# Optimization experiments

Measured on AMD Instinct MI355X. Metric: run time of the kernel, lower is better.

## Reference

```python
import jax, jax.numpy as jnp
import numpy as np

B, L = 4, 1024
V, D, H, NL = 32000, 256, 4, 8
S, DC, DI, NTYPES = 16, 4, 512, 5  # d_state, d_conv, d_inner=expand*d_model
NM, NA = 6, 2  # mamba blocks (layers 0,1,2,4,5,6), attention blocks (layers 3,7)


def layernorm(x, g, b):
    m = x.mean(-1, keepdims=True)
    v = x.var(-1, keepdims=True)
    return (x - m) / jnp.sqrt(v + 1e-5) * g + b


def mamba_block(x, g, b, in_w, conv_w, conv_b, xproj_w, dt_w, dt_b, A_log, Dp, out_w):
    res = x
    xn = layernorm(x, g, b)
    xz = xn @ in_w.T                          # [B,L,2*DI]
    xb, z = jnp.split(xz, 2, axis=-1)
    # depthwise causal conv1d (torch pads both sides then truncates to L == left-pad only)
    xc = jnp.transpose(xb, (0, 2, 1))         # [B,DI,L]
    xc = jax.lax.conv_general_dilated(xc, conv_w, (1,), [(DC - 1, 0)], feature_group_count=DI)
    xc = xc + conv_b[None, :, None]
    xb = jax.nn.silu(jnp.transpose(xc, (0, 2, 1)))  # [B,L,DI]
    A = -jnp.exp(A_log)                        # [DI,S]
    Bm, Cm = jnp.split(xb @ xproj_w.T, 2, axis=-1)  # each [B,L,S]
    dt = jax.nn.softplus(xb @ dt_w.T + dt_b)   # [B,L,DI]

    def step(h, inp):
        dt_t, B_t, C_t, x_t = inp              # [B,DI],[B,S],[B,S],[B,DI]
        A_bar = jnp.exp(dt_t[:, :, None] * A)  # [B,DI,S]
        h = A_bar * h + (dt_t * x_t)[:, :, None] * B_t[:, None, :]
        y = (h * C_t[:, None, :]).sum(-1) + Dp * x_t
        return h, y

    h0 = jnp.zeros((x.shape[0], DI, S), x.dtype)
    xs = (jnp.swapaxes(dt, 0, 1), jnp.swapaxes(Bm, 0, 1), jnp.swapaxes(Cm, 0, 1), jnp.swapaxes(xb, 0, 1))
    _, ys = jax.lax.scan(step, h0, xs)         # ys: [L,B,DI]
    y = jnp.swapaxes(ys, 0, 1) * jax.nn.silu(z)
    return y @ out_w.T + res


def attn_block(x, ts, mask, g, b, qkv_w, out_w, decay, ffg, ffb, ff1, ff2):
    Bs, Lq, Dm = x.shape
    dh = Dm // H
    res = x
    xn = layernorm(x, g, b)
    qkv = (xn @ qkv_w.T).reshape(Bs, Lq, 3, H, dh)
    q, k, v = qkv[:, :, 0], qkv[:, :, 1], qkv[:, :, 2]   # [B,L,H,dh]
    attn = jnp.einsum('bqhd,bkhd->bhqk', q, k) * dh ** -0.5
    t_diff = jnp.abs(ts[:, :, None] - ts[:, None, :])[:, None] / 24.0   # [B,1,L,L]
    attn = attn - jax.nn.softplus(decay)[None, :, None, None] * t_diff
    causal = jnp.triu(jnp.ones((Lq, Lq), bool), 1)
    attn = jnp.where(causal[None, None], -jnp.inf, attn)
    attn = jnp.where((mask == 0)[:, None, None, :], -jnp.inf, attn)
    attn = jax.nn.softmax(attn, axis=-1)       # dropout inactive (eval)
    out = jnp.einsum('bhqk,bkhd->bqhd', attn, v).reshape(Bs, Lq, Dm)
    x = res + out @ out_w.T
    xn2 = layernorm(x, ffg, ffb)
    return x + jax.nn.silu(xn2 @ ff1.T) @ ff2.T


def setup_inputs():
    key = jax.random.key(0)
    ks = iter(jax.random.split(key, 64))
    rn = lambda shape, s=0.02: jax.random.normal(next(ks), shape, jnp.float32) * s
    A_init = jnp.log(jnp.tile(jnp.arange(1, S + 1, dtype=jnp.float32)[None, None, :], (NM, DI, 1)))
    return dict(
        token_ids=jax.random.randint(next(ks), (B, L), 0, V, jnp.int32),
        token_types=jax.random.randint(next(ks), (B, L), 0, NTYPES, jnp.int32),
        timestamps=jax.random.uniform(next(ks), (B, L), jnp.float32) * 100.0,
        attention_mask=jnp.ones((B, L), jnp.int32),
        tok_emb=rn((V, D)).at[0].set(0.0),  # padding_idx=0
        type_emb=rn((NTYPES, D)),
        te_freq=rn((D // 2,), 0.01), te_phase=jnp.zeros((D // 2,)),
        te_w=rn((D, D)), te_b=jnp.zeros((D,)),
        m_norm_g=jnp.ones((NM, D)), m_norm_b=jnp.zeros((NM, D)),
        m_in_w=rn((NM, 2 * DI, D)),
        m_conv_w=rn((NM, DI, 1, DC)), m_conv_b=jnp.zeros((NM, DI)),
        m_xproj_w=rn((NM, 2 * S, DI)),
        m_dt_w=rn((NM, DI, DI)), m_dt_b=jnp.zeros((NM, DI)),
        m_Alog=A_init, m_D=jnp.ones((NM, DI)),
        m_out_w=rn((NM, D, DI)),
        a_norm_g=jnp.ones((NA, D)), a_norm_b=jnp.zeros((NA, D)),
        a_qkv_w=rn((NA, 3 * D, D)), a_out_w=rn((NA, D, D)),
        a_decay=jnp.full((NA, H), 0.01, jnp.float32),
        a_ffg=jnp.ones((NA, D)), a_ffb=jnp.zeros((NA, D)),
        a_ff1=rn((NA, 4 * D, D)), a_ff2=rn((NA, D, 4 * D)),
        f_g=jnp.ones((D,)), f_b=jnp.zeros((D,)),
        lm_w=rn((V, D)),
        re_w=rn((1, D)), re_b=jnp.zeros((1,)),
        mo_w=rn((1, D)), mo_b=jnp.zeros((1,)),
    )


def reference(token_ids, token_types, timestamps, attention_mask,
              tok_emb, type_emb, te_freq, te_phase, te_w, te_b,
              m_norm_g, m_norm_b, m_in_w, m_conv_w, m_conv_b, m_xproj_w,
              m_dt_w, m_dt_b, m_Alog, m_D, m_out_w,
              a_norm_g, a_norm_b, a_qkv_w, a_out_w, a_decay, a_ffg, a_ffb, a_ff1, a_ff2,
              f_g, f_b, lm_w, re_w, re_b, mo_w, mo_b):
    t = timestamps[..., None]
    freq = jax.nn.softplus(te_freq)
    enc = jnp.concatenate([jnp.sin(t * freq + te_phase), jnp.cos(t * freq + te_phase)], -1) @ te_w.T + te_b
    x = tok_emb[token_ids] + type_emb[token_types] + enc
    mi = ai = 0
    for i in range(NL):
        if (i + 1) % 4 == 0:
            x = attn_block(x, timestamps, attention_mask,
                           a_norm_g[ai], a_norm_b[ai], a_qkv_w[ai], a_out_w[ai], a_decay[ai],
                           a_ffg[ai], a_ffb[ai], a_ff1[ai], a_ff2[ai])
            ai += 1
        else:
            x = mamba_block(x, m_norm_g[mi], m_norm_b[mi], m_in_w[mi], m_conv_w[mi], m_conv_b[mi],
                            m_xproj_w[mi], m_dt_w[mi], m_dt_b[mi], m_Alog[mi], m_D[mi], m_out_w[mi])
            mi += 1
    x = layernorm(x, f_g, f_b)
    cls = x[:, 0, :]
    lm_logits = x @ lm_w.T
    readm = (cls @ re_w.T + re_b)[:, 0]
    mort = (cls @ mo_w.T + mo_b)[:, 0]
    return lm_logits, readm, mort
```

## Files before the change

kernel.cpp:

```cpp
#include <hip/hip_runtime.h>
#include <hip/hip_bf16.h>
#include <math.h>

#define BB 4
#define LL 1024
#define BL (BB*LL)
#define DD 256
#define VV 32000
#define HH 4
#define DH 64
#define SS 16
#define DCC 4
#define DII 512

typedef float f32x4 __attribute__((ext_vector_type(4)));
typedef short bh8  __attribute__((ext_vector_type(8)));
typedef unsigned short u16;

__device__ __forceinline__ float sp_f(float x) {
    return fmaxf(x, 0.f) + log1pf(expf(-fabsf(x)));
}
__device__ __forceinline__ float silu_f(float x) {
    return x / (1.f + expf(-x));
}
__device__ __forceinline__ short f2bf(float f) {
    __hip_bfloat16 h = __float2bfloat16(f);
    short s; __builtin_memcpy(&s, &h, 2); return s;
}
__device__ __forceinline__ float bf2f(u16 u) {
    unsigned v = ((unsigned)u) << 16;
    float f; __builtin_memcpy(&f, &v, 4); return f;
}

#define WB_TOT 5668864
#define LM_TOT 8192000
__global__ void cvtall_k(const float* __restrict__ te_w, const float* __restrict__ a_qkv,
                         const float* __restrict__ a_out, const float* __restrict__ a_ff1,
                         const float* __restrict__ a_ff2, const float* __restrict__ m_in,
                         const float* __restrict__ m_out, const float* __restrict__ m_dt,
                         const float* __restrict__ m_xp, const float* __restrict__ lm,
                         u16* __restrict__ dst, u16* __restrict__ dlm) {
    long i = ((long)blockIdx.x * 256 + threadIdx.x) * 4;
    const float* src; long off; u16* d; long doff;
    if (i >= WB_TOT) {
        long j = i - WB_TOT;
        if (j >= LM_TOT) return;
        src = lm; off = j; d = dlm; doff = j;
    } else {
        d = dst; doff = i;
        if      (i < 65536)   { src = te_w;  off = i; }
        else if (i < 458752)  { src = a_qkv; off = i - 65536; }
        else if (i < 589824)  { src = a_out; off = i - 458752; }
        else if (i < 1114112) { src = a_ff1; off = i - 589824; }
        else if (i < 1638400) { src = a_ff2; off = i - 1114112; }
        else if (i < 3211264) { src = m_in;  off = i - 1638400; }
        else if (i < 3997696) { src = m_out; off = i - 3211264; }
        else {
            long l = i - 3997696;
            int mi = (int)(l / 278528);
            long r = l - (long)mi * 278528;
            if (r < 262144) { src = m_dt + (long)mi * 262144; off = r; }
            else            { src = m_xp + (long)mi * 16384;  off = r - 262144; }
        }
    }
    float4 v = *(const float4*)(src + off);
    ushort4 u;
    u.x = (u16)f2bf(v.x); u.y = (u16)f2bf(v.y);
    u.z = (u16)f2bf(v.z); u.w = (u16)f2bf(v.w);
    *(ushort4*)(d + doff) = u;
}

__global__ void feat_k(const float* __restrict__ ts, const float* __restrict__ freq,
                       const float* __restrict__ phase, u16* __restrict__ feat) {
    int row = blockIdx.x, t = threadIdx.x;
    float tv = ts[row];
    int d = t & 127;
    float f = sp_f(freq[d]);
    float arg = tv * f + phase[d];
    feat[(size_t)row * DD + t] = (u16)f2bf((t < 128) ? sinf(arg) : cosf(arg));
}

__global__ void ln_k(const float* __restrict__ x, const float* __restrict__ g,
                     const float* __restrict__ bbias, u16* __restrict__ out) {
    __shared__ float red[8];
    int row = blockIdx.x, t = threadIdx.x;
    float v = x[(size_t)row * DD + t];
    float s = v;
    #pragma unroll
    for (int o = 32; o >= 1; o >>= 1) s += __shfl_xor(s, o);
    if ((t & 63) == 0) red[t >> 6] = s;
    __syncthreads();
    float mean = (red[0] + red[1] + red[2] + red[3]) * (1.f / 256.f);
    float d = v - mean;
    float s2 = d * d;
    #pragma unroll
    for (int o = 32; o >= 1; o >>= 1) s2 += __shfl_xor(s2, o);
    if ((t & 63) == 0) red[4 + (t >> 6)] = s2;
    __syncthreads();
    float var = (red[4] + red[5] + red[6] + red[7]) * (1.f / 256.f);
    out[(size_t)row * DD + t] = (u16)f2bf(d * rsqrtf(var + 1e-5f) * g[t] + bbias[t]);
}

template <int ACT, bool BOUT, bool VT>
__global__ __launch_bounds__(256) void lngemm_k(
    const float* __restrict__ X, const float* __restrict__ g, const float* __restrict__ bb,
    const u16* __restrict__ W, void* __restrict__ outv, u16* __restrict__ vt,
    int M, int N) {
    __shared__ __align__(16) char Abf[32768];
    __shared__ __align__(16) char Ws[8192];
    __shared__ float gs[256], bs[256];
    int tid = threadIdx.x;
    int bm = blockIdx.y * 64, bn = blockIdx.x * 64;
    gs[tid] = g[tid]; bs[tid] = bb[tid];

    int row = tid >> 2, part = tid & 3;
    const float* xr = X + (size_t)(bm + row) * 256 + part * 64;
    float4 vv[16];
    float s = 0.f, sq = 0.f;
    #pragma unroll
    for (int i = 0; i < 16; ++i) {
        vv[i] = *(const float4*)(xr + i * 4);
        s  += vv[i].x + vv[i].y + vv[i].z + vv[i].w;
        sq += vv[i].x * vv[i].x + vv[i].y * vv[i].y + vv[i].z * vv[i].z + vv[i].w * vv[i].w;
    }
    s += __shfl_xor(s, 1);  s += __shfl_xor(s, 2);
    sq += __shfl_xor(sq, 1); sq += __shfl_xor(sq, 2);
    float mean = s * (1.f / 256.f);
    float rstd = rsqrtf(sq * (1.f / 256.f) - mean * mean + 1e-5f);
    __syncthreads();
    #pragma unroll
    for (int i8 = 0; i8 < 8; ++i8) {
        bh8 p;
        #pragma unroll
        for (int j = 0; j < 8; ++j) {
            int e = i8 * 8 + j;
            float v = (j & 3) == 0 ? vv[e >> 2].x : (j & 3) == 1 ? vv[e >> 2].y
                    : (j & 3) == 2 ? vv[e >> 2].z : vv[e >> 2].w;
            int c = part * 64 + e;
            p[j] = f2bf((v - mean) * rstd * gs[c] + bs[c]);
        }
        *(bh8*)(Abf + (unsigned)((row * 512 + part * 128 + i8 * 16) ^ ((row & 7) << 4))) = p;
    }
    __syncthreads();

    int lane = tid & 63, wv = tid >> 6;
    int wm = wv >> 1, wn = wv & 1;
    int ro = lane & 15, kg = lane >> 4;
    f32x4 acc[2][2];
    #pragma unroll
    for (int i = 0; i < 2; ++i)
        #pragma unroll
        for (int j = 0; j < 2; ++j) acc[i][j] = (f32x4){0.f, 0.f, 0.f, 0.f};

    const u16* gw = W + (size_t)(bn + row) * 256 + part * 16;
    bool wvalid = (bn + row) < N;
    unsigned swb = (unsigned)(row * 128 + part * 32);
    unsigned sx  = (unsigned)((row & 7) << 4);
    for (int kk = 0; kk < 256; kk += 64) {
        if (kk) __syncthreads();
        bh8 w0 = {}, w1 = {};
        if (wvalid) { w0 = *(const bh8*)(gw + kk); w1 = *(const bh8*)(gw + kk + 8); }
        *(bh8*)(Ws + (swb ^ sx)) = w0;
        *(bh8*)(Ws + ((swb + 16) ^ sx)) = w1;
        __syncthreads();
        #pragma unroll
        for (int ks = 0; ks < 2; ++ks) {
            bh8 af[2], bf_[2];
            #pragma unroll
            for (int m = 0; m < 2; ++m) {
                int r = wm * 32 + m * 16 + ro;
                af[m] = *(const bh8*)(Abf + (unsigned)((r * 512 + kk * 2 + ks * 64 + kg * 16) ^ ((r & 7) << 4)));
            }
            #pragma unroll
            for (int n = 0; n < 2; ++n) {
                int r = wn * 32 + n * 16 + ro;
                bf_[n] = *(const bh8*)(Ws + (unsigned)((r * 128 + ks * 64 + kg * 16) ^ ((r & 7) << 4)));
            }
            #pragma unroll
            for (int m = 0; m < 2; ++m)
                #pragma unroll
                for (int n = 0; n < 2; ++n)
                    acc[m][n] = __builtin_amdgcn_mfma_f32_16x16x32_bf16(af[m], bf_[n], acc[m][n], 0, 0, 0);
        }
    }

    float* outf = (float*)outv;
    u16*   outb = (u16*)outv;
    int cr = (lane >> 4) * 4, cc = lane & 15;
    #pragma unroll
    for (int mf = 0; mf < 2; ++mf) {
        #pragma unroll
        for (int nf = 0; nf < 2; ++nf) {
            int n = bn + wn * 32 + nf * 16 + cc;
            if (n >= N) continue;
            int mbase = bm + wm * 32 + mf * 16 + cr;
            f32x4 a = acc[mf][nf];
            #pragma unroll
            for (int r = 0; r < 4; ++r) {
                float v = a[r];
                if (ACT == 1) v = silu_f(v);
                if (BOUT) outb[(size_t)(mbase + r) * N + n] = (u16)f2bf(v);
                else      outf[(size_t)(mbase + r) * N + n] = v;
            }
            if (VT && n >= 512) {
                int hh = (n - 512) >> 6, dd = (n - 512) & 63;
                int b_ = mbase >> 10, l = mbase & 1023;
                ushort4 uv;
                uv.x = (u16)f2bf(acc[mf][nf][0]); uv.y = (u16)f2bf(acc[mf][nf][1]);
                uv.z = (u16)f2bf(acc[mf][nf][2]); uv.w = (u16)f2bf(acc[mf][nf][3]);
                *(ushort4*)(vt + ((((size_t)b_ * HH + hh) * DH + dd) << 10) + l) = uv;
            }
        }
    }
}

template <int ACT, bool HASB, bool HASR, bool BOUT>
__global__ __launch_bounds__(256) void bgemm_k(
    const u16* __restrict__ A, const u16* __restrict__ W,
    const float* __restrict__ bias, const float* __restrict__ res,
    void* __restrict__ outv, float* __restrict__ out2, int M, int N, int K) {
    __shared__ __align__(16) char lds[16384];
    char* As = lds;
    char* Ws = lds + 8192;
    int tid = threadIdx.x;
    int bm = blockIdx.y * 64, bn = blockIdx.x * 64;
    int row = tid >> 2, q = tid & 3;
    int lane = tid & 63, wv = tid >> 6;
    int wm = wv >> 1, wn = wv & 1;
    int ro = lane & 15, kg = lane >> 4;

    f32x4 acc[2][2];
    #pragma unroll
    for (int i = 0; i < 2; ++i)
        #pragma unroll
        for (int j = 0; j < 2; ++j) acc[i][j] = (f32x4){0.f, 0.f, 0.f, 0.f};

    const u16* ga = A + (size_t)(bm + row) * K + q * 16;
    const u16* gw = W + (size_t)(bn + row) * K + q * 16;
    bool wvalid = (bn + row) < N;
    unsigned swb = (unsigned)(row * 128 + q * 32);
    unsigned sx  = (unsigned)((row & 7) << 4);

    for (int kk = 0; kk < K; kk += 64) {
        if (kk) __syncthreads();
        {
            *(bh8*)(As + (swb ^ sx)) = *(const bh8*)(ga);
            *(bh8*)(As + ((swb + 16) ^ sx)) = *(const bh8*)(ga + 8);
            bh8 w0 = {}, w1 = {};
            if (wvalid) { w0 = *(const bh8*)(gw); w1 = *(const bh8*)(gw + 8); }
            *(bh8*)(Ws + (swb ^ sx)) = w0;
            *(bh8*)(Ws + ((swb + 16) ^ sx)) = w1;
        }
        ga += 64; gw += 64;
        __syncthreads();
        #pragma unroll
        for (int ks = 0; ks < 2; ++ks) {
            bh8 af[2], bf_[2];
            #pragma unroll
            for (int m = 0; m < 2; ++m) {
                int r = wm * 32 + m * 16 + ro;
                af[m] = *(const bh8*)(As + (unsigned)((r * 128 + ks * 64 + kg * 16) ^ ((r & 7) << 4)));
            }
            #pragma unroll
            for (int n = 0; n < 2; ++n) {
                int r = wn * 32 + n * 16 + ro;
                bf_[n] = *(const bh8*)(Ws + (unsigned)((r * 128 + ks * 64 + kg * 16) ^ ((r & 7) << 4)));
            }
            #pragma unroll
            for (int m = 0; m < 2; ++m)
                #pragma unroll
                for (int n = 0; n < 2; ++n)
                    acc[m][n] = __builtin_amdgcn_mfma_f32_16x16x32_bf16(af[m], bf_[n], acc[m][n], 0, 0, 0);
        }
    }

    float* outf = (float*)outv;
    u16*   outb = (u16*)outv;
    int cr = (lane >> 4) * 4, cc = lane & 15;
    #pragma unroll
    for (int mf = 0; mf < 2; ++mf) {
        #pragma unroll
        for (int nf = 0; nf < 2; ++nf) {
            int n = bn + wn * 32 + nf * 16 + cc;
            if (n >= N) continue;
            int mbase = bm + wm * 32 + mf * 16 + cr;
            f32x4 a = acc[mf][nf];
            #pragma unroll
            for (int r = 0; r < 4; ++r) {
                float v = a[r];
                int m = mbase + r;
                if (ACT == 3) {
                    if (n < 512) outf[(size_t)m * 512 + n] = sp_f(v + bias[n]);
                    else         out2[(size_t)m * 32 + (n - 512)] = v;
                } else {
                    if (HASB) v += bias[n];
                    if (ACT == 1) v = silu_f(v);
                    if (HASR) v += res[(size_t)m * N + n];
                    if (BOUT) outb[(size_t)m * N + n] = (u16)f2bf(v);
                    else      outf[(size_t)m * N + n] = v;
                }
            }
        }
    }
}

template <int ACT, bool HASB, bool HASR>
__global__ __launch_bounds__(512) void bgemmsk_k(
    const u16* __restrict__ A, const u16* __restrict__ W,
    const float* __restrict__ bias, const float* __restrict__ res,
    float* __restrict__ out, int M, int N, int K,
    const int* __restrict__ ids, const int* __restrict__ typ,
    const float* __restrict__ tok, const float* __restrict__ tpe) {
    __shared__ __align__(16) char As[2][8192];
    __shared__ __align__(16) char Ws[2][8192];
    __shared__ float red[4][32][33];
    int tid = threadIdx.x;
    int kh = tid >> 8;
    int t  = tid & 255;
    int bm = blockIdx.y * 64, bn = blockIdx.x * 64;
    int row = t >> 2, q = t & 3;
    int lane = tid & 63;
    int wq = (tid >> 6) & 3;
    int wm = wq >> 1, wn = wq & 1;
    int ro = lane & 15, kg = lane >> 4;

    f32x4 acc[2][2];
    #pragma unroll
    for (int i = 0; i < 2; ++i)
        #pragma unroll
        for (int j = 0; j < 2; ++j) acc[i][j] = (f32x4){0.f, 0.f, 0.f, 0.f};

    int khalf = K >> 1;
    const u16* ga = A + (size_t)(bm + row) * K + kh * khalf + q * 16;
    const u16* gw = W + (size_t)(bn + row) * K + kh * khalf + q * 16;
    unsigned swb = (unsigned)(row * 128 + q * 32);
    unsigned sx  = (unsigned)((row & 7) << 4);

    for (int kk = 0; kk < khalf; kk += 64) {
        if (kk) __syncthreads();
        *(bh8*)(As[kh] + (swb ^ sx)) = *(const bh8*)(ga);
        *(bh8*)(As[kh] + ((swb + 16) ^ sx)) = *(const bh8*)(ga + 8);
        *(bh8*)(Ws[kh] + (swb ^ sx)) = *(const bh8*)(gw);
        *(bh8*)(Ws[kh] + ((swb + 16) ^ sx)) = *(const bh8*)(gw + 8);
        ga += 64; gw += 64;
        __syncthreads();
        #pragma unroll
        for (int ks = 0; ks < 2; ++ks) {
            bh8 af[2], bf_[2];
            #pragma unroll
            for (int m = 0; m < 2; ++m) {
                int r = wm * 32 + m * 16 + ro;
                af[m] = *(const bh8*)(As[kh] + (unsigned)((r * 128 + ks * 64 + kg * 16) ^ ((r & 7) << 4)));
            }
            #pragma unroll
            for (int n = 0; n < 2; ++n) {
                int r = wn * 32 + n * 16 + ro;
                bf_[n] = *(const bh8*)(Ws[kh] + (unsigned)((r * 128 + ks * 64 + kg * 16) ^ ((r & 7) << 4)));
            }
            #pragma unroll
            for (int m = 0; m < 2; ++m)
                #pragma unroll
                for (int n = 0; n < 2; ++n)
                    acc[m][n] = __builtin_amdgcn_mfma_f32_16x16x32_bf16(af[m], bf_[n], acc[m][n], 0, 0, 0);
        }
    }

    int cr = (lane >> 4) * 4, cc = lane & 15;
    __syncthreads();
    if (kh == 1) {
        #pragma unroll
        for (int mf = 0; mf < 2; ++mf)
            #pragma unroll
            for (int nf = 0; nf < 2; ++nf)
                #pragma unroll
                for (int r = 0; r < 4; ++r)
                    red[wq][mf * 16 + cr + r][nf * 16 + cc] = acc[mf][nf][r];
    }
    __syncthreads();
    if (kh == 0) {
        #pragma unroll
        for (int mf = 0; mf < 2; ++mf) {
            #pragma unroll
            for (int nf = 0; nf < 2; ++nf) {
                int n = bn + wn * 32 + nf * 16 + cc;
                if (n >= N) continue;
                int mbase = bm + wm * 32 + mf * 16 + cr;
                #pragma unroll
                for (int r = 0; r < 4; ++r) {
                    float v = acc[mf][nf][r] + red[wq][mf * 16 + cr + r][nf * 16 + cc];
                    int m = mbase + r;
                    if (ACT == 4) {
                        v += bias[n] + tok[(size_t)ids[m] * DD + n] + tpe[(size_t)typ[m] * DD + n];
                    } else {
                        if (HASB) v += bias[n];
                        if (HASR) v += res[(size_t)m * N + n];
                    }
                    out[(size_t)m * N + n] = v;
                }
            }
        }
    }
}

__global__ __launch_bounds__(256) void mgemmL_k(
    const u16* __restrict__ A, const u16* __restrict__ W,
    float* __restrict__ out, int M, int N, int K) {
    __shared__ __align__(16) char lds[32768];
    char* As = lds;
    char* Ws = lds + 16384;
    int lid = blockIdx.y * 32 + blockIdx.x;
    int xcd = lid & 7, wk = lid >> 3;
    int nt = xcd * 32 + (wk >> 5);
    int mt = wk & 31;
    if (nt * 128 >= N) return;
    int bm = mt * 128, bn = nt * 128;

    int tid = threadIdx.x;
    int row = tid >> 1, half = tid & 1;
    int lane = tid & 63, wv = tid >> 6;
    int wm = wv >> 1, wn = wv & 1;
    int ro = lane & 15, kg = lane >> 4;

    f32x4 acc[4][4];
    #pragma unroll
    for (int i = 0; i < 4; ++i)
        #pragma unroll
        for (int j = 0; j < 4; ++j) acc[i][j] = (f32x4){0.f, 0.f, 0.f, 0.f};

    const u16* ga = A + (size_t)(bm + row) * K + half * 32;
    const u16* gw = W + (size_t)(bn + row) * K + half * 32;
    unsigned swb = (unsigned)(row * 128 + half * 64);
    unsigned sx  = (unsigned)((row & 7) << 4);

    for (int kk = 0; kk < K; kk += 64) {
        if (kk) __syncthreads();
        #pragma unroll
        for (int j = 0; j < 4; ++j) {
            *(bh8*)(As + ((swb + j * 16) ^ sx)) = *(const bh8*)(ga + j * 8);
            *(bh8*)(Ws + ((swb + j * 16) ^ sx)) = *(const bh8*)(gw + j * 8);
        }
        ga += 64; gw += 64;
        __syncthreads();
        #pragma unroll
        for (int ks = 0; ks < 2; ++ks) {
            bh8 af[4], bf_[4];
            #pragma unroll
            for (int m = 0; m < 4; ++m) {
                int r = wm * 64 + m * 16 + ro;
                af[m] = *(const bh8*)(As + (unsigned)((r * 128 + ks * 64 + kg * 16) ^ ((r & 7) << 4)));
            }
            #pragma unroll
            for (int n = 0; n < 4; ++n) {
                int r = wn * 64 + n * 16 + ro;
                bf_[n] = *(const bh8*)(Ws + (unsigned)((r * 128 + ks * 64 + kg * 16) ^ ((r & 7) << 4)));
            }
            #pragma unroll
            for (int m = 0; m < 4; ++m)
                #pragma unroll
                for (int n = 0; n < 4; ++n)
                    acc[m][n] = __builtin_amdgcn_mfma_f32_16x16x32_bf16(af[m], bf_[n], acc[m][n], 0, 0, 0);
        }
    }

    int cr = (lane >> 4) * 4, cc = lane & 15;
    #pragma unroll
    for (int mf = 0; mf < 4; ++mf) {
        #pragma unroll
        for (int nf = 0; nf < 4; ++nf) {
            int n = bn + wn * 64 + nf * 16 + cc;
            int mbase = bm + wm * 64 + mf * 16 + cr;
            f32x4 a = acc[mf][nf];
            #pragma unroll
            for (int r = 0; r < 4; ++r)
                out[(size_t)(mbase + r) * N + n] = a[r];
        }
    }
}

__global__ void conv_k(const u16* __restrict__ xz, const float* __restrict__ w,
                       const float* __restrict__ cb, u16* __restrict__ xbb) {
    int idx = blockIdx.x * blockDim.x + threadIdx.x;
    int c = idx & (DII - 1);
    int row = idx >> 9;
    int l = row & (LL - 1);
    int base = row - l;
    const float* wc = w + c * DCC;
    float s = cb[c];
    #pragma unroll
    for (int j = 0; j < DCC; ++j) {
        int ll = l - (DCC - 1) + j;
        if (ll >= 0) s = fmaf(wc[j], bf2f(xz[((size_t)(base + ll)) * (2 * DII) + c]), s);
    }
    xbb[(size_t)idx] = (u16)f2bf(silu_f(s));
}

__global__ __launch_bounds__(256) void scan_k(
    const float* __restrict__ dt,
    const u16* __restrict__ xb,
    const float* __restrict__ bc,
    const u16* __restrict__ xz,
    const float* __restrict__ Alog, const float* __restrict__ Dp,
    u16* __restrict__ y) {
    __shared__ float pa[SS][257];
    __shared__ float ph[SS][257];
    int di = blockIdx.x & (DII - 1);
    int b  = blockIdx.x >> 9;
    int t  = threadIdx.x;
    int l0 = t * 4;
    size_t rb = (size_t)(b * LL + l0);

    float A[SS];
    #pragma unroll
    for (int s = 0; s < SS; ++s) A[s] = -expf(Alog[di * SS + s]);

    float dtv[4], xv[4];
    #pragma unroll
    for (int j = 0; j < 4; ++j) {
        dtv[j] = dt[(rb + j) * DII + di];
        xv[j]  = bf2f(xb[(rb + j) * DII + di]);
    }

    float Pa[SS], Ph[SS];
    #pragma unroll
    for (int j = 0; j < 4; ++j) {
        float u = dtv[j] * xv[j];
        const float* bt = bc + (rb + j) * (2 * SS);
        #pragma unroll
        for (int s = 0; s < SS; ++s) {
            float a = expf(dtv[j] * A[s]);
            float w = u * bt[s];
            if (j == 0) { Pa[s] = a; Ph[s] = w; }
            else        { Pa[s] *= a; Ph[s] = fmaf(a, Ph[s], w); }
        }
    }
    #pragma unroll
    for (int s = 0; s < SS; ++s) { pa[s][t] = Pa[s]; ph[s][t] = Ph[s]; }
    __syncthreads();

    #pragma unroll
    for (int off = 1; off < 256; off <<= 1) {
        float qa[SS], qh[SS];
        bool has = (t >= off);
        if (has) {
            #pragma unroll
            for (int s = 0; s < SS; ++s) { qa[s] = pa[s][t - off]; qh[s] = ph[s][t - off]; }
        }
        __syncthreads();
        if (has) {
            #pragma unroll
            for (int s = 0; s < SS; ++s) {
                ph[s][t] = fmaf(pa[s][t], qh[s], ph[s][t]);
                pa[s][t] *= qa[s];
            }
        }
        __syncthreads();
    }

    float h[SS];
    if (t == 0) {
        #pragma unroll
        for (int s = 0; s < SS; ++s) h[s] = 0.f;
    } else {
        #pragma unroll
        for (int s = 0; s < SS; ++s) h[s] = ph[s][t - 1];
    }
    float Dv = Dp[di];
    #pragma unroll
    for (int j = 0; j < 4; ++j) {
        float u = dtv[j] * xv[j];
        const float* bt = bc + (rb + j) * (2 * SS);
        float acc = 0.f;
        #pragma unroll
        for (int s = 0; s < SS; ++s) {
            float a = expf(dtv[j] * A[s]);
            h[s] = fmaf(a, h[s], u * bt[s]);
            acc = fmaf(h[s], bt[SS + s], acc);
        }
        float zv = bf2f(xz[(rb + j) * (2 * DII) + DII + di]);
        y[(rb + j) * DII + di] = (u16)f2bf(fmaf(Dv, xv[j], acc) * silu_f(zv));
    }
}

__global__ __launch_bounds__(256) void fattn_k(
    const u16* __restrict__ qkv, const u16* __restrict__ vt,
    const float* __restrict__ ts, const int* __restrict__ mask,
    const float* __restrict__ decay, u16* __restrict__ out) {
    __shared__ __align__(16) char ksm[8192];
    __shared__ __align__(16) char vsm[8192];
    __shared__ __align__(16) char psm[8192];
    __shared__ float tsk[64];
    __shared__ int   msk[64];

    int tid = threadIdx.x;
    int lane = tid & 63, wvi = tid >> 6;
    int qt = blockIdx.x & 15;
    int h  = (blockIdx.x >> 4) & 3;
    int b  = blockIdx.x >> 6;
    int q0 = qt * 64;
    int g = lane >> 4, c = lane & 15;

    bh8 qf[2];
    {
        const u16* qrow = qkv + ((size_t)(b * LL + q0 + wvi * 16 + c)) * (3 * DD) + h * DH;
        qf[0] = *(const bh8*)(qrow + g * 8);
        qf[1] = *(const bh8*)(qrow + 32 + g * 8);
    }
    float tq[4];
    #pragma unroll
    for (int j = 0; j < 4; ++j) tq[j] = ts[b * LL + q0 + wvi * 16 + g * 4 + j];
    float spd = sp_f(decay[h]);

    f32x4 o[4];
    #pragma unroll
    for (int n = 0; n < 4; ++n) o[n] = (f32x4){0.f, 0.f, 0.f, 0.f};
    float mrow[4] = {-INFINITY, -INFINITY, -INFINITY, -INFINITY};
    float drow[4] = {0.f, 0.f, 0.f, 0.f};

    char* pw = psm + wvi * 2048;

    for (int kt = 0; kt <= qt; ++kt) {
        int k0 = kt * 64;
        __syncthreads();
        {
            int row = tid >> 2, qq = tid & 3;
            unsigned sw = (unsigned)((row & 7) << 4);
            unsigned base = (unsigned)(row * 128 + qq * 32);
            const u16* kr = qkv + ((size_t)(b * LL + k0 + row)) * (3 * DD) + DD + h * DH + qq * 16;
            *(bh8*)(ksm + (base ^ sw)) = *(const bh8*)(kr);
            *(bh8*)(ksm + ((base + 16) ^ sw)) = *(const bh8*)(kr + 8);
            const u16* vr = vt + ((((size_t)b * HH + h) * DH + row) << 10) + k0 + qq * 16;
            *(bh8*)(vsm + (base ^ sw)) = *(const bh8*)(vr);
            *(bh8*)(vsm + ((base + 16) ^ sw)) = *(const bh8*)(vr + 8);
            if (tid < 64) { tsk[tid] = ts[b * LL + k0 + tid]; msk[tid] = mask[b * LL + k0 + tid]; }
        }
        __syncthreads();

        f32x4 sf[4];
        #pragma unroll
        for (int n = 0; n < 4; ++n) sf[n] = (f32x4){0.f, 0.f, 0.f, 0.f};
        #pragma unroll
        for (int ks = 0; ks < 2; ++ks) {
            #pragma unroll
            for (int nf = 0; nf < 4; ++nf) {
                int rr = nf * 16 + c;
                bh8 kf = *(const bh8*)(ksm + (unsigned)((rr * 128 + ks * 64 + g * 16) ^ ((rr & 7) << 4)));
                sf[nf] = __builtin_amdgcn_mfma_f32_16x16x32_bf16(qf[ks], kf, sf[nf], 0, 0, 0);
            }
        }
        float mnew[4] = {mrow[0], mrow[1], mrow[2], mrow[3]};
        #pragma unroll
        for (int nf = 0; nf < 4; ++nf) {
            int kk = c + 16 * nf;
            float tk = tsk[kk];
            bool md = (msk[kk] == 0);
            #pragma unroll
            for (int j = 0; j < 4; ++j) {
                int qrow = q0 + wvi * 16 + g * 4 + j;
                float s = sf[nf][j] * 0.125f - spd * fabsf(tq[j] - tk) * (1.f / 24.f);
                bool dead = md || (k0 + kk > qrow);
                s = dead ? -INFINITY : s;
                sf[nf][j] = s;
                mnew[j] = fmaxf(mnew[j], s);
            }
        }
        #pragma unroll
        for (int off = 1; off <= 8; off <<= 1)
            #pragma unroll
            for (int j = 0; j < 4; ++j) mnew[j] = fmaxf(mnew[j], __shfl_xor(mnew[j], off));
        float scl[4], psum[4];
        #pragma unroll
        for (int j = 0; j < 4; ++j) {
            scl[j] = (mnew[j] == -INFINITY) ? 1.f : expf(mrow[j] - mnew[j]);
            psum[j] = 0.f;
            mrow[j] = mnew[j];
        }
        #pragma unroll
        for (int nf = 0; nf < 4; ++nf) {
            #pragma unroll
            for (int j = 0; j < 4; ++j) {
                float s = sf[nf][j];
                float p = (s == -INFINITY) ? 0.f : expf(s - mrow[j]);
                psum[j] += p;
                int row = g * 4 + j;
                *(short*)(pw + (unsigned)((row * 128 + (c + 16 * nf) * 2) ^ ((row & 7) << 4))) = f2bf(p);
            }
        }
        #pragma unroll
        for (int off = 1; off <= 8; off <<= 1)
            #pragma unroll
            for (int j = 0; j < 4; ++j) psum[j] += __shfl_xor(psum[j], off);
        #pragma unroll
        for (int j = 0; j < 4; ++j) drow[j] = drow[j] * scl[j] + psum[j];
        #pragma unroll
        for (int n = 0; n < 4; ++n)
            #pragma unroll
            for (int j = 0; j < 4; ++j) o[n][j] *= scl[j];
        #pragma unroll
        for (int ks = 0; ks < 2; ++ks) {
            bh8 pf = *(const bh8*)(pw + (unsigned)((c * 128 + ks * 64 + g * 16) ^ ((c & 7) << 4)));
            #pragma unroll
            for (int n = 0; n < 4; ++n) {
                int rr = n * 16 + c;
                bh8 vf = *(const bh8*)(vsm + (unsigned)((rr * 128 + ks * 64 + g * 16) ^ ((rr & 7) << 4)));
                o[n] = __builtin_amdgcn_mfma_f32_16x16x32_bf16(pf, vf, o[n], 0, 0, 0);
            }
        }
    }
    #pragma unroll
    for (int n = 0; n < 4; ++n) {
        #pragma unroll
        for (int j = 0; j < 4; ++j) {
            int qrow = q0 + wvi * 16 + g * 4 + j;
            out[((size_t)(b * LL + qrow)) * DD + h * DH + c + 16 * n] = (u16)f2bf(o[n][j] / drow[j]);
        }
    }
}

__global__ __launch_bounds__(64) void heads_k(
    const u16* __restrict__ xn, const float* __restrict__ re_w, const float* __restrict__ re_b,
    const float* __restrict__ mo_w, const float* __restrict__ mo_b, float* __restrict__ out) {
    int lane = threadIdx.x;
    int b = blockIdx.x & 3;
    int which = blockIdx.x >> 2;
    const float* wv = which ? mo_w : re_w;
    const u16* row = xn + (size_t)b * LL * DD;
    float s = 0.f;
    #pragma unroll
    for (int d = 0; d < DD / 64; ++d) s = fmaf(bf2f(row[lane + d * 64]), wv[lane + d * 64], s);
    #pragma unroll
    for (int o = 32; o >= 1; o >>= 1) s += __shfl_xor(s, o);
    if (lane == 0) out[(size_t)VV * BL + which * 4 + b] = s + (which ? mo_b[0] : re_b[0]);
}

extern "C" void kernel_launch(void* const* d_in, const int* in_sizes, int n_in,
                              void* d_out, int out_size, void* d_ws, size_t ws_size,
                              hipStream_t stream) {
    const int*   ids      = (const int*)  d_in[0];
    const int*   typ      = (const int*)  d_in[1];
    const float* ts       = (const float*)d_in[2];
    const int*   amask    = (const int*)  d_in[3];
    const float* tok_emb  = (const float*)d_in[4];
    const float* type_emb = (const float*)d_in[5];
    const float* te_freq  = (const float*)d_in[6];
    const float* te_phase = (const float*)d_in[7];
    const float* te_w     = (const float*)d_in[8];
    const float* te_b     = (const float*)d_in[9];
    const float* m_norm_g = (const float*)d_in[10];
    const float* m_norm_b = (const float*)d_in[11];
    const float* m_in_w   = (const float*)d_in[12];
    const float* m_conv_w = (const float*)d_in[13];
    const float* m_conv_b = (const float*)d_in[14];
    const float* m_xproj  = (const float*)d_in[15];
    const float* m_dt_w   = (const float*)d_in[16];
    const float* m_dt_b   = (const float*)d_in[17];
    const float* m_Alog   = (const float*)d_in[18];
    const float* m_D      = (const float*)d_in[19];
    const float* m_out_w  = (const float*)d_in[20];
    const float* a_norm_g = (const float*)d_in[21];
    const float* a_norm_b = (const float*)d_in[22];
    const float* a_qkv_w  = (const float*)d_in[23];
    const float* a_out_w  = (const float*)d_in[24];
    const float* a_decay  = (const float*)d_in[25];
    const float* a_ffg    = (const float*)d_in[26];
    const float* a_ffb    = (const float*)d_in[27];
    const float* a_ff1    = (const float*)d_in[28];
    const float* a_ff2    = (const float*)d_in[29];
    const float* f_g      = (const float*)d_in[30];
    const float* f_b      = (const float*)d_in[31];
    const float* lm_w     = (const float*)d_in[32];
    const float* re_w     = (const float*)d_in[33];
    const float* re_b     = (const float*)d_in[34];
    const float* mo_w     = (const float*)d_in[35];
    const float* mo_b     = (const float*)d_in[36];

    float* out = (float*)d_out;
    float* ws  = (float*)d_ws;

    float* x    = ws;
    u16*   xnb  = (u16*)(ws + 1048576);
    u16*   t1   = (u16*)(ws + 1572864);
    u16*   b1   = (u16*)(ws + 3670016);
    u16*   b2   = (u16*)(ws + 5767168);
    float* t3   = ws + 6815744;
    float* t5   = ws + 8912896;
    u16*   vtb  = (u16*)(ws + 9043968);
    u16*   wbuf = (u16*)(ws + 9568256);
    u16*   wlm  = (u16*)(ws + 12402688);

    const u16* w_te  = wbuf;
    const u16* w_qkv = wbuf + 65536;
    const u16* w_ao  = wbuf + 458752;
    const u16* w_ff1 = wbuf + 589824;
    const u16* w_ff2 = wbuf + 1114112;
    const u16* w_min = wbuf + 1638400;
    const u16* w_mo  = wbuf + 3211264;
    const u16* w_dtx = wbuf + 3997696;

    cvtall_k<<<(WB_TOT + LM_TOT) / 1024, 256, 0, stream>>>(
        te_w, a_qkv_w, a_out_w, a_ff1, a_ff2, m_in_w, m_out_w, m_dt_w, m_xproj, lm_w, wbuf, wlm);
    feat_k<<<BL, 256, 0, stream>>>(ts, te_freq, te_phase, b1);
    bgemmsk_k<4, true, false><<<dim3(4, BL / 64), 512, 0, stream>>>(
        b1, w_te, te_b, nullptr, x, BL, DD, DD, ids, typ, tok_emb, type_emb);

    int mi = 0, ai = 0;
    for (int i = 0; i < 8; ++i) {
        if ((i + 1) % 4 == 0) {
            lngemm_k<0, true, true><<<dim3(12, BL / 64), 256, 0, stream>>>(
                x, a_norm_g + ai * DD, a_norm_b + ai * DD,
                w_qkv + (size_t)ai * 196608, t1, vtb, BL, 3 * DD);
            fattn_k<<<BB * HH * (LL / 64), 256, 0, stream>>>(
                t1, vtb, ts, amask, a_decay + ai * HH, b1);
            bgemmsk_k<0, false, true><<<dim3(4, BL / 64), 512, 0, stream>>>(
                b1, w_ao + (size_t)ai * 65536, nullptr, x, x, BL, DD, DD,
                nullptr, nullptr, nullptr, nullptr);
            lngemm_k<1, true, false><<<dim3(16, BL / 64), 256, 0, stream>>>(
                x, a_ffg + ai * DD, a_ffb + ai * DD,
                w_ff1 + (size_t)ai * 262144, b1, nullptr, BL, 4 * DD);
            bgemmsk_k<0, false, true><<<dim3(4, BL / 64), 512, 0, stream>>>(
                b1, w_ff2 + (size_t)ai * 262144, nullptr, x, x, BL, DD, 4 * DD,
                nullptr, nullptr, nullptr, nullptr);
            ++ai;
        } else {
            lngemm_k<0, true, false><<<dim3(16, BL / 64), 256, 0, stream>>>(
                x, m_norm_g + mi * DD, m_norm_b + mi * DD,
                w_min + (size_t)mi * 262144, t1, nullptr, BL, 2 * DII);
            conv_k<<<(BL * DII) / 256, 256, 0, stream>>>(
                t1, m_conv_w + (size_t)mi * DII * DCC, m_conv_b + mi * DII, b1);
            bgemm_k<3, true, false, false><<<dim3(9, BL / 64), 256, 0, stream>>>(
                b1, w_dtx + (size_t)mi * 278528, m_dt_b + mi * DII, nullptr, t3, t5, BL, 544, DII);
            scan_k<<<BB * DII, 256, 0, stream>>>(
                t3, b1, t5, t1, m_Alog + (size_t)mi * DII * SS, m_D + mi * DII, b2);
            bgemmsk_k<0, false, true><<<dim3(4, BL / 64), 512, 0, stream>>>(
                b2, w_mo + (size_t)mi * 131072, nullptr, x, x, BL, DD, DII,
                nullptr, nullptr, nullptr, nullptr);
            ++mi;
        }
    }

    ln_k<<<BL, 256, 0, stream>>>(x, f_g, f_b, xnb);
    mgemmL_k<<<dim3(32, 256), 256, 0, stream>>>(xnb, wlm, out, BL, VV, DD);
    heads_k<<<8, 64, 0, stream>>>(xnb, re_w, re_b, mo_w, mo_b, out);
}
```

Before: 1.446 ms.

## Replace split-K small GEMM with 32-row tiles and split attention keys across two groups

The split-K 512-thread GEMM used for the N=256 projections becomes a plain 256-thread kernel with 32x64 tiles, so twice as many blocks launch and the LDS reduction is gone. The flash-attention kernel moves to 512 threads, with two 256-thread groups taking alternating key tiles into double LDS buffers. Their partial softmax states are then merged through shared memory. This targets low occupancy and long serial key loops for causal query tiles, at the cost of more LDS, an extra merge step, and idle groups on odd tile counts.

```diff
diff --git a/kernel.cpp b/kernel.cpp
--- a/kernel.cpp
+++ b/kernel.cpp
@@ -305,99 +305,69 @@
 }
 
 template <int ACT, bool HASB, bool HASR>
-__global__ __launch_bounds__(512) void bgemmsk_k(
+__global__ __launch_bounds__(256) void bgemm32_k(
     const u16* __restrict__ A, const u16* __restrict__ W,
     const float* __restrict__ bias, const float* __restrict__ res,
     float* __restrict__ out, int M, int N, int K,
     const int* __restrict__ ids, const int* __restrict__ typ,
     const float* __restrict__ tok, const float* __restrict__ tpe) {
-    __shared__ __align__(16) char As[2][8192];
-    __shared__ __align__(16) char Ws[2][8192];
-    __shared__ float red[4][32][33];
+    __shared__ __align__(16) char As[4096];
+    __shared__ __align__(16) char Ws[8192];
     int tid = threadIdx.x;
-    int kh = tid >> 8;
-    int t  = tid & 255;
-    int bm = blockIdx.y * 64, bn = blockIdx.x * 64;
-    int row = t >> 2, q = t & 3;
-    int lane = tid & 63;
-    int wq = (tid >> 6) & 3;
-    int wm = wq >> 1, wn = wq & 1;
+    int bm = blockIdx.y * 32, bn = blockIdx.x * 64;
+    int lane = tid & 63, wv = tid >> 6;
+    int wm = wv >> 1, wn = wv & 1;
     int ro = lane & 15, kg = lane >> 4;
 
-    f32x4 acc[2][2];
-    #pragma unroll
-    for (int i = 0; i < 2; ++i)
-        #pragma unroll
-        for (int j = 0; j < 2; ++j) acc[i][j] = (f32x4){0.f, 0.f, 0.f, 0.f};
-
-    int khalf = K >> 1;
-    const u16* ga = A + (size_t)(bm + row) * K + kh * khalf + q * 16;
-    const u16* gw = W + (size_t)(bn + row) * K + kh * khalf + q * 16;
-    unsigned swb = (unsigned)(row * 128 + q * 32);
-    unsigned sx  = (unsigned)((row & 7) << 4);
-
-    for (int kk = 0; kk < khalf; kk += 64) {
+    f32x4 acc[2];
+    acc[0] = (f32x4){0.f, 0.f, 0.f, 0.f};
+    acc[1] = (f32x4){0.f, 0.f, 0.f, 0.f};
+
+    int arow = tid >> 3, aq = tid & 7;
+    const u16* ga = A + (size_t)(bm + arow) * K + aq * 8;
+    unsigned aswb = (unsigned)(arow * 128 + aq * 16);
+    unsigned asx  = (unsigned)((arow & 7) << 4);
+    int wrow = tid >> 2, wq = tid & 3;
+    const u16* gw = W + (size_t)(bn + wrow) * K + wq * 16;
+    unsigned wswb = (unsigned)(wrow * 128 + wq * 32);
+    unsigned wsx  = (unsigned)((wrow & 7) << 4);
+
+    for (int kk = 0; kk < K; kk += 64) {
         if (kk) __syncthreads();
-        *(bh8*)(As[kh] + (swb ^ sx)) = *(const bh8*)(ga);
-        *(bh8*)(As[kh] + ((swb + 16) ^ sx)) = *(const bh8*)(ga + 8);
-        *(bh8*)(Ws[kh] + (swb ^ sx)) = *(const bh8*)(gw);
-        *(bh8*)(Ws[kh] + ((swb + 16) ^ sx)) = *(const bh8*)(gw + 8);
+        *(bh8*)(As + (aswb ^ asx)) = *(const bh8*)(ga);
+        *(bh8*)(Ws + (wswb ^ wsx)) = *(const bh8*)(gw);
+        *(bh8*)(Ws + ((wswb + 16) ^ wsx)) = *(const bh8*)(gw + 8);
         ga += 64; gw += 64;
         __syncthreads();
         #pragma unroll
         for (int ks = 0; ks < 2; ++ks) {
-            bh8 af[2], bf_[2];
-            #pragma unroll
-            for (int m = 0; m < 2; ++m) {
-                int r = wm * 32 + m * 16 + ro;
-                af[m] = *(const bh8*)(As[kh] + (unsigned)((r * 128 + ks * 64 + kg * 16) ^ ((r & 7) << 4)));
-            }
+            int r = wm * 16 + ro;
+            bh8 af = *(const bh8*)(As + (unsigned)((r * 128 + ks * 64 + kg * 16) ^ ((r & 7) << 4)));
             #pragma unroll
             for (int n = 0; n < 2; ++n) {
-                int r = wn * 32 + n * 16 + ro;
-                bf_[n] = *(const bh8*)(Ws[kh] + (unsigned)((r * 128 + ks * 64 + kg * 16) ^ ((r & 7) << 4)));
-            }
-            #pragma unroll
-            for (int m = 0; m < 2; ++m)
-                #pragma unroll
-                for (int n = 0; n < 2; ++n)
-                    acc[m][n] = __builtin_amdgcn_mfma_f32_16x16x32_bf16(af[m], bf_[n], acc[m][n], 0, 0, 0);
+                int rr = wn * 32 + n * 16 + ro;
+                bh8 bf_ = *(const bh8*)(Ws + (unsigned)((rr * 128 + ks * 64 + kg * 16) ^ ((rr & 7) << 4)));
+                acc[n] = __builtin_amdgcn_mfma_f32_16x16x32_bf16(af, bf_, acc[n], 0, 0, 0);
+            }
         }
     }
 
     int cr = (lane >> 4) * 4, cc = lane & 15;
-    __syncthreads();
-    if (kh == 1) {
-        #pragma unroll
-        for (int mf = 0; mf < 2; ++mf)
-            #pragma unroll
-            for (int nf = 0; nf < 2; ++nf)
-                #pragma unroll
-                for (int r = 0; r < 4; ++r)
-                    red[wq][mf * 16 + cr + r][nf * 16 + cc] = acc[mf][nf][r];
-    }
-    __syncthreads();
-    if (kh == 0) {
-        #pragma unroll
-        for (int mf = 0; mf < 2; ++mf) {
-            #pragma unroll
-            for (int nf = 0; nf < 2; ++nf) {
-                int n = bn + wn * 32 + nf * 16 + cc;
-                if (n >= N) continue;
-                int mbase = bm + wm * 32 + mf * 16 + cr;
-                #pragma unroll
-                for (int r = 0; r < 4; ++r) {
-                    float v = acc[mf][nf][r] + red[wq][mf * 16 + cr + r][nf * 16 + cc];
-                    int m = mbase + r;
-                    if (ACT == 4) {
-                        v += bias[n] + tok[(size_t)ids[m] * DD + n] + tpe[(size_t)typ[m] * DD + n];
-                    } else {
-                        if (HASB) v += bias[n];
-                        if (HASR) v += res[(size_t)m * N + n];
-                    }
-                    out[(size_t)m * N + n] = v;
-                }
-            }
+    #pragma unroll
+    for (int nf = 0; nf < 2; ++nf) {
+        int n = bn + wn * 32 + nf * 16 + cc;
+        int mbase = bm + wm * 16 + cr;
+        #pragma unroll
+        for (int r = 0; r < 4; ++r) {
+            float v = acc[nf][r];
+            int m = mbase + r;
+            if (ACT == 4) {
+                v += bias[n] + tok[(size_t)ids[m] * DD + n] + tpe[(size_t)typ[m] * DD + n];
+            } else {
+                if (HASB) v += bias[n];
+                if (HASR) v += res[(size_t)m * N + n];
+            }
+            out[(size_t)m * N + n] = v;
         }
     }
 }
@@ -495,10 +465,8 @@
 }
 
 __global__ __launch_bounds__(256) void scan_k(
-    const float* __restrict__ dt,
-    const u16* __restrict__ xb,
-    const float* __restrict__ bc,
-    const u16* __restrict__ xz,
+    const float* __restrict__ dt, const u16* __restrict__ xb,
+    const float* __restrict__ bc, const u16* __restrict__ xz,
     const float* __restrict__ Alog, const float* __restrict__ Dp,
     u16* __restrict__ y) {
     __shared__ float pa[SS][257];
@@ -581,18 +549,22 @@
     }
 }
 
-__global__ __launch_bounds__(256) void fattn_k(
+__global__ __launch_bounds__(512) void fattn_k(
     const u16* __restrict__ qkv, const u16* __restrict__ vt,
     const float* __restrict__ ts, const int* __restrict__ mask,
     const float* __restrict__ decay, u16* __restrict__ out) {
-    __shared__ __align__(16) char ksm[8192];
-    __shared__ __align__(16) char vsm[8192];
-    __shared__ __align__(16) char psm[8192];
-    __shared__ float tsk[64];
-    __shared__ int   msk[64];
+    __shared__ __align__(16) char ksm[2][8192];
+    __shared__ __align__(16) char vsm[2][8192];
+    __shared__ __align__(16) char psm[16384];
+    __shared__ float mrg[256][25];
+    __shared__ float tsk[2][64];
+    __shared__ int   msk[2][64];
 
     int tid = threadIdx.x;
-    int lane = tid & 63, wvi = tid >> 6;
+    int grp = tid >> 8;
+    int lt  = tid & 255;
+    int lane = tid & 63;
+    int wvi = (tid >> 6) & 3;
     int qt = blockIdx.x & 15;
     int h  = (blockIdx.x >> 4) & 3;
     int b  = blockIdx.x >> 6;
@@ -616,24 +588,28 @@
     float mrow[4] = {-INFINITY, -INFINITY, -INFINITY, -INFINITY};
     float drow[4] = {0.f, 0.f, 0.f, 0.f};
 
-    char* pw = psm + wvi * 2048;
-
-    for (int kt = 0; kt <= qt; ++kt) {
+    char* pw = psm + (tid >> 6) * 2048;
+
+    int nt = (qt + 2) >> 1;
+    for (int it = 0; it < nt; ++it) {
+        int kt = it * 2 + grp;
+        bool act = (kt <= qt);
         int k0 = kt * 64;
         __syncthreads();
-        {
-            int row = tid >> 2, qq = tid & 3;
+        if (act) {
+            int row = lt >> 2, qq = lt & 3;
             unsigned sw = (unsigned)((row & 7) << 4);
             unsigned base = (unsigned)(row * 128 + qq * 32);
             const u16* kr = qkv + ((size_t)(b * LL + k0 + row)) * (3 * DD) + DD + h * DH + qq * 16;
-            *(bh8*)(ksm + (base ^ sw)) = *(const bh8*)(kr);
-            *(bh8*)(ksm + ((base + 16) ^ sw)) = *(const bh8*)(kr + 8);
+            *(bh8*)(ksm[grp] + (base ^ sw)) = *(const bh8*)(kr);
+            *(bh8*)(ksm[grp] + ((base + 16) ^ sw)) = *(const bh8*)(kr + 8);
             const u16* vr = vt + ((((size_t)b * HH + h) * DH + row) << 10) + k0 + qq * 16;
-            *(bh8*)(vsm + (base ^ sw)) = *(const bh8*)(vr);
-            *(bh8*)(vsm + ((base + 16) ^ sw)) = *(const bh8*)(vr + 8);
-            if (tid < 64) { tsk[tid] = ts[b * LL + k0 + tid]; msk[tid] = mask[b * LL + k0 + tid]; }
+            *(bh8*)(vsm[grp] + (base ^ sw)) = *(const bh8*)(vr);
+            *(bh8*)(vsm[grp] + ((base + 16) ^ sw)) = *(const bh8*)(vr + 8);
+            if (lt < 64) { tsk[grp][lt] = ts[b * LL + k0 + lt]; msk[grp][lt] = mask[b * LL + k0 + lt]; }
         }
         __syncthreads();
+        if (!act) continue;
 
         f32x4 sf[4];
         #pragma unroll
@@ -643,7 +619,7 @@
             #pragma unroll
             for (int nf = 0; nf < 4; ++nf) {
                 int rr = nf * 16 + c;
-                bh8 kf = *(const bh8*)(ksm + (unsigned)((rr * 128 + ks * 64 + g * 16) ^ ((rr & 7) << 4)));
+                bh8 kf = *(const bh8*)(ksm[grp] + (unsigned)((rr * 128 + ks * 64 + g * 16) ^ ((rr & 7) << 4)));
                 sf[nf] = __builtin_amdgcn_mfma_f32_16x16x32_bf16(qf[ks], kf, sf[nf], 0, 0, 0);
             }
         }
@@ -651,8 +627,8 @@
         #pragma unroll
         for (int nf = 0; nf < 4; ++nf) {
             int kk = c + 16 * nf;
-            float tk = tsk[kk];
-            bool md = (msk[kk] == 0);
+            float tk = tsk[grp][kk];
+            bool md = (msk[grp][kk] == 0);
             #pragma unroll
             for (int j = 0; j < 4; ++j) {
                 int qrow = q0 + wvi * 16 + g * 4 + j;
@@ -701,17 +677,43 @@
             #pragma unroll
             for (int n = 0; n < 4; ++n) {
                 int rr = n * 16 + c;
-                bh8 vf = *(const bh8*)(vsm + (unsigned)((rr * 128 + ks * 64 + g * 16) ^ ((rr & 7) << 4)));
+                bh8 vf = *(const bh8*)(vsm[grp] + (unsigned)((rr * 128 + ks * 64 + g * 16) ^ ((rr & 7) << 4)));
                 o[n] = __builtin_amdgcn_mfma_f32_16x16x32_bf16(pf, vf, o[n], 0, 0, 0);
             }
         }
     }
-    #pragma unroll
-    for (int n = 0; n < 4; ++n) {
+
+    __syncthreads();
+    if (grp == 1) {
+        float* m_ = mrg[lt];
+        #pragma unroll
+        for (int j = 0; j < 4; ++j) { m_[j] = mrow[j]; m_[4 + j] = drow[j]; }
+        #pragma unroll
+        for (int n = 0; n < 4; ++n)
+            #pragma unroll
+            for (int j = 0; j < 4; ++j) m_[8 + n * 4 + j] = o[n][j];
+    }
+    __syncthreads();
+    if (grp == 0) {
+        float* m_ = mrg[lt];
         #pragma unroll
         for (int j = 0; j < 4; ++j) {
-            int qrow = q0 + wvi * 16 + g * 4 + j;
-            out[((size_t)(b * LL + qrow)) * DD + h * DH + c + 16 * n] = (u16)f2bf(o[n][j] / drow[j]);
+            float m1 = m_[j], d1 = m_[4 + j];
+            float mm = fmaxf(mrow[j], m1);
+            float s0 = (mrow[j] == -INFINITY) ? 0.f : expf(mrow[j] - mm);
+            float s1 = (m1 == -INFINITY) ? 0.f : expf(m1 - mm);
+            drow[j] = drow[j] * s0 + d1 * s1;
+            #pragma unroll
+            for (int n = 0; n < 4; ++n)
+                o[n][j] = o[n][j] * s0 + m_[8 + n * 4 + j] * s1;
+        }
+        #pragma unroll
+        for (int n = 0; n < 4; ++n) {
+            #pragma unroll
+            for (int j = 0; j < 4; ++j) {
+                int qrow = q0 + wvi * 16 + g * 4 + j;
+                out[((size_t)(b * LL + qrow)) * DD + h * DH + c + 16 * n] = (u16)f2bf(o[n][j] / drow[j]);
+            }
         }
     }
 }
@@ -799,7 +801,7 @@
     cvtall_k<<<(WB_TOT + LM_TOT) / 1024, 256, 0, stream>>>(
         te_w, a_qkv_w, a_out_w, a_ff1, a_ff2, m_in_w, m_out_w, m_dt_w, m_xproj, lm_w, wbuf, wlm);
     feat_k<<<BL, 256, 0, stream>>>(ts, te_freq, te_phase, b1);
-    bgemmsk_k<4, true, false><<<dim3(4, BL / 64), 512, 0, stream>>>(
+    bgemm32_k<4, true, false><<<dim3(4, BL / 32), 256, 0, stream>>>(
         b1, w_te, te_b, nullptr, x, BL, DD, DD, ids, typ, tok_emb, type_emb);
 
     int mi = 0, ai = 0;
@@ -808,15 +810,15 @@
             lngemm_k<0, true, true><<<dim3(12, BL / 64), 256, 0, stream>>>(
                 x, a_norm_g + ai * DD, a_norm_b + ai * DD,
                 w_qkv + (size_t)ai * 196608, t1, vtb, BL, 3 * DD);
-            fattn_k<<<BB * HH * (LL / 64), 256, 0, stream>>>(
+            fattn_k<<<BB * HH * (LL / 64), 512, 0, stream>>>(
                 t1, vtb, ts, amask, a_decay + ai * HH, b1);
-            bgemmsk_k<0, false, true><<<dim3(4, BL / 64), 512, 0, stream>>>(
+            bgemm32_k<0, false, true><<<dim3(4, BL / 32), 256, 0, stream>>>(
                 b1, w_ao + (size_t)ai * 65536, nullptr, x, x, BL, DD, DD,
                 nullptr, nullptr, nullptr, nullptr);
             lngemm_k<1, true, false><<<dim3(16, BL / 64), 256, 0, stream>>>(
                 x, a_ffg + ai * DD, a_ffb + ai * DD,
                 w_ff1 + (size_t)ai * 262144, b1, nullptr, BL, 4 * DD);
-            bgemmsk_k<0, false, true><<<dim3(4, BL / 64), 512, 0, stream>>>(
+            bgemm32_k<0, false, true><<<dim3(4, BL / 32), 256, 0, stream>>>(
                 b1, w_ff2 + (size_t)ai * 262144, nullptr, x, x, BL, DD, 4 * DD,
                 nullptr, nullptr, nullptr, nullptr);
             ++ai;
@@ -830,7 +832,7 @@
                 b1, w_dtx + (size_t)mi * 278528, m_dt_b + mi * DII, nullptr, t3, t5, BL, 544, DII);
             scan_k<<<BB * DII, 256, 0, stream>>>(
                 t3, b1, t5, t1, m_Alog + (size_t)mi * DII * SS, m_D + mi * DII, b2);
-            bgemmsk_k<0, false, true><<<dim3(4, BL / 64), 512, 0, stream>>>(
+            bgemm32_k<0, false, true><<<dim3(4, BL / 32), 256, 0, stream>>>(
                 b2, w_mo + (size_t)mi * 131072, nullptr, x, x, BL, DD, DII,
                 nullptr, nullptr, nullptr, nullptr);
             ++mi;
```

Result: faster. 1.372 ms (-5.2%).
